# Kernel optimization log

Hardware: AMD Instinct MI355X
Metric: run time of the kernel (lower is better)

The kernel has to match this reference:

```python
import jax, jax.numpy as jnp
import numpy as np

D_MODEL = 2048
NUM_HEADS = 16
HEAD_DIM = D_MODEL // NUM_HEADS
SCALE = HEAD_DIM ** 0.5
B, TQ, CACHE_LEN = 4, 1024, 1024


def setup_inputs() -> dict:
    key = jax.random.key(0)
    ks = jax.random.split(key, 13)
    f = jnp.float32
    inp = {
        'query': jax.random.normal(ks[0], (B, TQ, D_MODEL), f),
        'key': jax.random.normal(ks[1], (B, TQ, D_MODEL), f),
        'value': jax.random.normal(ks[2], (B, TQ, D_MODEL), f),
        'cache_key': jax.random.normal(ks[3], (B, CACHE_LEN, D_MODEL), f),
        'cache_value': jax.random.normal(ks[4], (B, CACHE_LEN, D_MODEL), f),
        'Wq': jax.random.normal(ks[5], (D_MODEL, D_MODEL), f) * 0.02,
        'bq': jnp.zeros((D_MODEL,), f),
        'Wk': jax.random.normal(ks[6], (D_MODEL, D_MODEL), f) * 0.02,
        'bk': jnp.zeros((D_MODEL,), f),
        'Wv': jax.random.normal(ks[7], (D_MODEL, D_MODEL), f) * 0.02,
        'bv': jnp.zeros((D_MODEL,), f),
        'Wo': jax.random.normal(ks[8], (D_MODEL, D_MODEL), f) * 0.02,
        'bo': jnp.zeros((D_MODEL,), f),
    }
    return inp


def _split(x):
    b, t, _ = x.shape
    return jnp.transpose(x.reshape(b, t, NUM_HEADS, HEAD_DIM), (0, 2, 1, 3))  # [B,H,T,Dh]


def reference(query, key, value, cache_key, cache_value, Wq, bq, Wk, bk, Wv, bv, Wo, bo):
    b, tq, _ = query.shape
    Q = query @ Wq.T + bq
    K = key @ Wk.T + bk
    V = value @ Wv.T + bv
    # cache holds already-projected K/V; concat along time
    K = jnp.concatenate([cache_key, K], axis=1)
    V = jnp.concatenate([cache_value, V], axis=1)
    total = K.shape[1]
    Qh, Kh, Vh = _split(Q), _split(K), _split(V)  # [B,H,T,Dh]
    scores = jnp.einsum('bhqd,bhkd->bhqk', Qh, Kh) / SCALE  # [B,H,Tq,total]
    # faithful to original: tril(Tq, total) mask (row i sees cols 0..i)
    mask = jnp.tril(jnp.ones((tq, total), dtype=bool))
    scores = jnp.where(mask[None, None], scores, -jnp.inf)
    attn = jax.nn.softmax(scores, axis=-1)  # eval mode: no dropout
    out = jnp.einsum('bhqk,bhkd->bhqd', attn, Vh)
    out = jnp.transpose(out, (0, 2, 1, 3)).reshape(b, tq, D_MODEL)
    out = out @ Wo.T + bo
    # new cache: torch reshapes the transposed [B,H,T,Dh] tensor directly
    new_k = Kh.reshape(b, -1, D_MODEL)
    new_v = Vh.reshape(b, -1, D_MODEL)
    return out, new_k, new_v
```

## Files before the change

kernel.cpp:

```cpp
#include <hip/hip_runtime.h>
#include <hip/hip_bf16.h>


typedef __bf16 bf16x8 __attribute__((ext_vector_type(8)));
typedef unsigned short u16x8 __attribute__((ext_vector_type(8)));
typedef float  f32x4  __attribute__((ext_vector_type(4)));
typedef unsigned int u32;

#define MFMA16(a, b, c) __builtin_amdgcn_mfma_f32_16x16x32_bf16((a), (b), (c), 0, 0, 0)

__device__ __forceinline__ void async16(__bf16* lds_p, const __bf16* g) {
    __builtin_amdgcn_global_load_lds(
        (__attribute__((address_space(1))) void*)g,
        (__attribute__((address_space(3))) void*)lds_p, 16, 0, 0);
}

__global__ __launch_bounds__(256) void prep(
    const float* __restrict__ q, const float* __restrict__ k, const float* __restrict__ v,
    const float* __restrict__ wq, const float* __restrict__ wk,
    const float* __restrict__ wv, const float* __restrict__ wo,
    const float* __restrict__ ck, const float* __restrict__ cv,
    float* __restrict__ nk, float* __restrict__ nv,
    __bf16* __restrict__ dq, __bf16* __restrict__ dk, __bf16* __restrict__ dv,
    __bf16* __restrict__ dwq, __bf16* __restrict__ dwk,
    __bf16* __restrict__ dwv, __bf16* __restrict__ dwo,
    __bf16* __restrict__ ckb, __bf16* __restrict__ cvb) {
    const int nthreads = gridDim.x * blockDim.x;
    for (int i = blockIdx.x * blockDim.x + threadIdx.x; i < 7340032; i += nthreads) {
        if (i < 2097152) {
            const int sel = i >> 20;
            const int j = i & 1048575;
            const int dh8 = j & 15;
            const int t = (j >> 4) & 1023;
            const int h = (j >> 14) & 15;
            const int b = j >> 18;
            const float* src = sel ? cv : ck;
            float* dst = sel ? nv : nk;
            __bf16* dstb = sel ? cvb : ckb;
            const size_t si = ((size_t)(b << 10) + t) * 2048 + (h << 7) + (dh8 << 3);
            const size_t di = ((size_t)b << 22) + ((size_t)h << 18) + (t << 7) + (dh8 << 3);
            const size_t bi = (((size_t)(b * 16 + h) * 1024 + t) << 7) + (dh8 << 3);
            const f32x4 x0 = *(const f32x4*)&src[si];
            const f32x4 x1 = *(const f32x4*)&src[si + 4];
            *(f32x4*)&dst[di] = x0;
            *(f32x4*)&dst[di + 4] = x1;
            bf16x8 bx;
#pragma unroll
            for (int e = 0; e < 4; e++) {
                bx[e]     = (__bf16)x0[e];
                bx[e + 4] = (__bf16)x1[e];
            }
            *(bf16x8*)&dstb[bi] = bx;
        } else {
            const float* s;
            __bf16* d;
            int off;
            if (i < 5242880) {
                const int ii = i - 2097152;
                const int r = ii >> 20;
                off = ii & 1048575;
                s = (r == 0) ? q : (r == 1) ? k : v;
                d = (r == 0) ? dq : (r == 1) ? dk : dv;
            } else {
                const int ii = i - 5242880;
                const int r = ii >> 19;
                off = ii & 524287;
                s = (r == 0) ? wq : (r == 1) ? wk : (r == 2) ? wv : wo;
                d = (r == 0) ? dwq : (r == 1) ? dwk : (r == 2) ? dwv : dwo;
            }
            const f32x4 x0 = *(const f32x4*)(s + (size_t)off * 8);
            const f32x4 x1 = *(const f32x4*)(s + (size_t)off * 8 + 4);
            bf16x8 o;
#pragma unroll
            for (int j2 = 0; j2 < 4; j2++) {
                o[j2]     = (__bf16)x0[j2];
                o[j2 + 4] = (__bf16)x1[j2];
            }
            *(bf16x8*)(d + (size_t)off * 8) = o;
        }
    }
}

template <int MODE>
__global__ __launch_bounds__(512, 2) void gemm8(
    const __bf16* __restrict__ A,
    const __bf16* __restrict__ W0, const __bf16* __restrict__ W1,
    const __bf16* __restrict__ W2,
    const float* __restrict__ bz0, const float* __restrict__ bz1,
    const float* __restrict__ bz2,
    void* __restrict__ C0, float* __restrict__ C1, float* __restrict__ C2) {
    extern __shared__ __bf16 lds[];
    constexpr int K = 2048;
    const int tid = threadIdx.x;
    const int w = tid >> 6, lane = tid & 63;
    const int wm = w >> 2, wn = w & 3;
    const int g = lane >> 4, c = lane & 15;

    const int lin = blockIdx.x;
    const int nb = lin & 7, mb = lin >> 3;
    const int m0 = mb << 7, n0 = nb << 8;
    const int seg = (MODE == 1) ? (mb >> 5) : 0;
    const __bf16* W = (MODE == 0 || seg == 0) ? W0 : (seg == 1) ? W1 : W2;
    const float* bias = (MODE == 0) ? bz0 : (seg == 0) ? bz0 : (seg == 1) ? bz1 : bz2;

    const __bf16* Ab = A + (size_t)m0 * K;
    const __bf16* Wb = W + (size_t)n0 * K;

    const int srow = lane >> 2;
    const int sch = (lane & 3) ^ (((lane >> 5) & 1) << 1);
    const int foff = c * 32 + ((g ^ ((c >> 3) << 1)) << 3);

    f32x4 acc[4][4] = {};

    auto stgA = [&](int T, int rg) {
#pragma unroll
        for (int u = 0; u < 2; u++) {
            const __bf16* gs = Ab + (size_t)(w * 16 + srow) * K + T * 64 + u * 32 + sch * 8;
            async16(&lds[rg * 24576 + (w * 2 + u) * 512], gs);
        }
    };
    auto stgB = [&](int T, int rg) {
#pragma unroll
        for (int u = 0; u < 4; u++) {
            const int rowblk = 2 * w + (u >> 1), kk = u & 1;
            const __bf16* gs = Wb + (size_t)(rowblk * 16 + srow) * K + T * 64 + kk * 32 + sch * 8;
            async16(&lds[rg * 24576 + 8192 + (w * 4 + u) * 512], gs);
        }
    };

    stgA(0, 0); stgB(0, 0);
    stgA(1, 1); stgB(1, 1);
    asm volatile("s_waitcnt vmcnt(6)" ::: "memory");
    asm volatile("s_barrier" ::: "memory");

    int rg = 0;
    for (int T = 0; T < 32; T++) {
        int rs = rg + 2; if (rs >= 3) rs -= 3;
        const int base = rg * 24576;
        bf16x8 fa[4], fb[4];

#pragma unroll
        for (int mi = 0; mi < 4; mi++)
            fa[mi] = *(const bf16x8*)&lds[base + ((wm * 4 + mi) * 2 + 0) * 512 + foff];
#pragma unroll
        for (int ni = 0; ni < 4; ni++)
            fb[ni] = *(const bf16x8*)&lds[base + 8192 + ((wn * 4 + ni) * 2 + 0) * 512 + foff];
        if (T < 30) stgA(T + 2, rs);
        asm volatile("s_barrier" ::: "memory");
        asm volatile("s_waitcnt lgkmcnt(0)" ::: "memory");
        __builtin_amdgcn_sched_barrier(0);
        __builtin_amdgcn_s_setprio(1);
#pragma unroll
        for (int mi = 0; mi < 4; mi++)
#pragma unroll
            for (int ni = 0; ni < 4; ni++)
                acc[mi][ni] = MFMA16(fa[mi], fb[ni], acc[mi][ni]);
        __builtin_amdgcn_s_setprio(0);
        asm volatile("s_barrier" ::: "memory");

#pragma unroll
        for (int mi = 0; mi < 4; mi++)
            fa[mi] = *(const bf16x8*)&lds[base + ((wm * 4 + mi) * 2 + 1) * 512 + foff];
#pragma unroll
        for (int ni = 0; ni < 4; ni++)
            fb[ni] = *(const bf16x8*)&lds[base + 8192 + ((wn * 4 + ni) * 2 + 1) * 512 + foff];
        if (T < 30) {
            stgB(T + 2, rs);
            asm volatile("s_waitcnt vmcnt(6)" ::: "memory");
        } else {
            asm volatile("s_waitcnt vmcnt(0)" ::: "memory");
        }
        asm volatile("s_barrier" ::: "memory");
        asm volatile("s_waitcnt lgkmcnt(0)" ::: "memory");
        __builtin_amdgcn_sched_barrier(0);
        __builtin_amdgcn_s_setprio(1);
#pragma unroll
        for (int mi = 0; mi < 4; mi++)
#pragma unroll
            for (int ni = 0; ni < 4; ni++)
                acc[mi][ni] = MFMA16(fa[mi], fb[ni], acc[mi][ni]);
        __builtin_amdgcn_s_setprio(0);
        asm volatile("s_barrier" ::: "memory");

        rg = (rg + 1 == 3) ? 0 : rg + 1;
    }

#pragma unroll
    for (int ni = 0; ni < 4; ni++) {
        const int col = n0 + wn * 64 + ni * 16 + c;
        const float bv = bias[col];
        const int h = col >> 7, dh = col & 127;
#pragma unroll
        for (int mi = 0; mi < 4; mi++) {
            const int rowb = m0 + wm * 64 + mi * 16 + g * 4;
#pragma unroll
            for (int r = 0; r < 4; r++) {
                const float v = acc[mi][ni][r] + bv;
                if (MODE == 0) {
                    ((float*)C0)[(size_t)(rowb + r) * 2048 + col] = v;
                } else {
                    const int lrow = (rowb + r) & 4095;
                    const int b = lrow >> 10, t = lrow & 1023;
                    if (seg == 0)
                        ((__bf16*)C0)[(((size_t)(b * 16 + h) * 1024) + t) * 128 + dh] = (__bf16)v;
                    else if (seg == 1)
                        C1[(((size_t)(b * 16 + h) * 2048) + 1024 + t) * 128 + dh] = v;
                    else
                        C2[(((size_t)(b * 16 + h) * 2048) + 1024 + t) * 128 + dh] = v;
                }
            }
        }
    }
}

__global__ __launch_bounds__(128) void attn_k(const __bf16* __restrict__ Qw,
                                              const __bf16* __restrict__ cK,
                                              const __bf16* __restrict__ cV,
                                              __bf16* __restrict__ O) {
    __shared__ __bf16 Kt[32 * 128];
    __shared__ u32 Vt32[128 * 16];
    __shared__ __bf16 Pw[2][16 * 32];

    const int tid = threadIdx.x;
    const int w = tid >> 6;
    const int lane = tid & 63;
    const int g = lane >> 4, c = lane & 15;

    const int lin = blockIdx.x + (blockIdx.y << 4) + (blockIdx.z << 8);
    const int xcd = lin & 7;
    const int j = lin >> 3;
    const int bh = xcd * 8 + (j & 7);
    const int qq = j >> 3;
    const int c4 = qq & 3, m = qq >> 2;
    const int qb = ((m & 1) == 0) ? (c4 * 4 + (m >> 1)) : (31 - c4 * 4 - (m >> 1));
    const int b = bh >> 4, h = bh & 15;
    const int q0 = qb << 5;
    const float inv_scale = 0.08838834764831845f;

    const __bf16* qbase = Qw + (((size_t)bh * 1024) + q0 + w * 16) * 128;
    bf16x8 qf[4];
#pragma unroll
    for (int dc = 0; dc < 4; dc++)
        qf[dc] = *(const bf16x8*)&qbase[c * 128 + dc * 32 + g * 8];

    f32x4 accO[8] = {};
    float m_run[4], l_run[4];
#pragma unroll
    for (int r = 0; r < 4; r++) { m_run[r] = -1e30f; l_run[r] = 0.0f; }

    const int trips = qb + 1;
    const __bf16* kb = cK + (size_t)bh * 1024 * 128;
    const __bf16* vb = cV + (size_t)bh * 1024 * 128;

    const int skey = tid >> 2, sgrp = tid & 3;
    const int ss = skey & 7;
    const int kp = tid >> 3, dbv = tid & 7;

    for (int kt = 0; kt < trips; kt++) {
        const int k0 = kt * 32;
        const __bf16* kr = &kb[(size_t)(k0 + skey) * 128 + sgrp * 32];
        const bf16x8 k_a = *(const bf16x8*)&kr[0];
        const bf16x8 k_b = *(const bf16x8*)&kr[8];
        const bf16x8 k_c = *(const bf16x8*)&kr[16];
        const bf16x8 k_d = *(const bf16x8*)&kr[24];
        const __bf16* vr0 = &vb[(size_t)(k0 + 2 * kp) * 128 + dbv * 16];
        const __bf16* vr1 = &vb[(size_t)(k0 + 2 * kp + 1) * 128 + dbv * 16];
        const bf16x8 v0a = *(const bf16x8*)&vr0[0];
        const bf16x8 v0b = *(const bf16x8*)&vr0[8];
        const bf16x8 v1a = *(const bf16x8*)&vr1[0];
        const bf16x8 v1b = *(const bf16x8*)&vr1[8];
        __syncthreads();
        {
            const int c0 = sgrp * 4;
            *(bf16x8*)&Kt[skey * 128 + (((c0 + 0) ^ ss) << 3)] = k_a;
            *(bf16x8*)&Kt[skey * 128 + (((c0 + 1) ^ ss) << 3)] = k_b;
            *(bf16x8*)&Kt[skey * 128 + (((c0 + 2) ^ ss) << 3)] = k_c;
            *(bf16x8*)&Kt[skey * 128 + (((c0 + 3) ^ ss) << 3)] = k_d;
        }
        {
            const u16x8 a0 = __builtin_bit_cast(u16x8, v0a);
            const u16x8 a1 = __builtin_bit_cast(u16x8, v0b);
            const u16x8 b0 = __builtin_bit_cast(u16x8, v1a);
            const u16x8 b1 = __builtin_bit_cast(u16x8, v1b);
#pragma unroll
            for (int jj = 0; jj < 8; jj++) {
                const int d0 = dbv * 16 + jj;
                const int d1 = dbv * 16 + 8 + jj;
                const int pc0 = (((kp >> 2) ^ ((d0 >> 3) & 3)) << 2) | (kp & 3);
                const int pc1 = (((kp >> 2) ^ ((d1 >> 3) & 3)) << 2) | (kp & 3);
                Vt32[d0 * 16 + pc0] = (u32)a0[jj] | ((u32)b0[jj] << 16);
                Vt32[d1 * 16 + pc1] = (u32)a1[jj] | ((u32)b1[jj] << 16);
            }
        }
        __syncthreads();

        f32x4 s_acc[2] = {};
#pragma unroll
        for (int nt = 0; nt < 2; nt++) {
            const int krow = nt * 16 + c;
            const int ks = krow & 7;
#pragma unroll
            for (int dc = 0; dc < 4; dc++) {
                const bf16x8 kf =
                    *(const bf16x8*)&Kt[krow * 128 + (((dc * 4 + g) ^ ks) << 3)];
                s_acc[nt] = MFMA16(qf[dc], kf, s_acc[nt]);
            }
        }

        float p[2][4], alpha[4];
#pragma unroll
        for (int r = 0; r < 4; r++) {
            const int qrow = q0 + w * 16 + g * 4 + r;
            float s0 = (k0 + c      <= qrow) ? s_acc[0][r] * inv_scale : -1e30f;
            float s1 = (k0 + 16 + c <= qrow) ? s_acc[1][r] * inv_scale : -1e30f;
            float rm = fmaxf(s0, s1);
            rm = fmaxf(rm, __shfl_xor(rm, 1));
            rm = fmaxf(rm, __shfl_xor(rm, 2));
            rm = fmaxf(rm, __shfl_xor(rm, 4));
            rm = fmaxf(rm, __shfl_xor(rm, 8));
            const float mnew = fmaxf(m_run[r], rm);
            alpha[r] = __expf(m_run[r] - mnew);
            const float p0 = __expf(s0 - mnew);
            const float p1 = __expf(s1 - mnew);
            p[0][r] = p0; p[1][r] = p1;
            float ps = p0 + p1;
            ps += __shfl_xor(ps, 1);
            ps += __shfl_xor(ps, 2);
            ps += __shfl_xor(ps, 4);
            ps += __shfl_xor(ps, 8);
            l_run[r] = alpha[r] * l_run[r] + ps;
            m_run[r] = mnew;
        }
#pragma unroll
        for (int nt2 = 0; nt2 < 8; nt2++)
#pragma unroll
            for (int r = 0; r < 4; r++)
                accO[nt2][r] *= alpha[r];

#pragma unroll
        for (int nt = 0; nt < 2; nt++)
#pragma unroll
            for (int r = 0; r < 4; r++)
                Pw[w][(g * 4 + r) * 32 + ((((nt << 1) | (c >> 3)) ^ g) << 3) + (c & 7)] =
                    (__bf16)p[nt][r];
        asm volatile("s_waitcnt lgkmcnt(0)" ::: "memory");
        __builtin_amdgcn_sched_barrier(0);

        const bf16x8 pf = *(const bf16x8*)&Pw[w][c * 32 + ((g ^ ((c >> 2) & 3)) << 3)];
#pragma unroll
        for (int nt2 = 0; nt2 < 8; nt2++) {
            const int vrow = nt2 * 16 + c;
            const bf16x8 vf = *(const bf16x8*)&(
                (const __bf16*)Vt32)[vrow * 32 + ((g ^ ((vrow >> 3) & 3)) << 3)];
            accO[nt2] = MFMA16(pf, vf, accO[nt2]);
        }
    }

#pragma unroll
    for (int nt2 = 0; nt2 < 8; nt2++)
#pragma unroll
        for (int r = 0; r < 4; r++) {
            const float v = accO[nt2][r] / l_run[r];
            const int row = b * 1024 + q0 + w * 16 + g * 4 + r;
            const int col = h * 128 + nt2 * 16 + c;
            O[(size_t)row * 2048 + col] = (__bf16)v;
        }
}

extern "C" void kernel_launch(void* const* d_in, const int* in_sizes, int n_in,
                              void* d_out, int out_size, void* d_ws, size_t ws_size,
                              hipStream_t stream) {
    const float* query       = (const float*)d_in[0];
    const float* key         = (const float*)d_in[1];
    const float* value       = (const float*)d_in[2];
    const float* cache_key   = (const float*)d_in[3];
    const float* cache_value = (const float*)d_in[4];
    const float* Wq = (const float*)d_in[5];
    const float* bq = (const float*)d_in[6];
    const float* Wk = (const float*)d_in[7];
    const float* bk = (const float*)d_in[8];
    const float* Wv = (const float*)d_in[9];
    const float* bv = (const float*)d_in[10];
    const float* Wo = (const float*)d_in[11];
    const float* bo = (const float*)d_in[12];

    float* out   = (float*)d_out;
    float* new_k = out + 8388608;
    float* new_v = out + 25165824;

    __bf16* p = (__bf16*)d_ws;
    __bf16* ws_q    = p; p += 8388608;
    __bf16* ws_attn = p; p += 8388608;
    __bf16* q_bf    = p; p += 8388608;
    __bf16* k_bf    = p; p += 8388608;
    __bf16* v_bf    = p; p += 8388608;
    __bf16* wq_bf   = p; p += 4194304;
    __bf16* wk_bf   = p; p += 4194304;
    __bf16* wv_bf   = p; p += 4194304;
    __bf16* wo_bf   = p; p += 4194304;
    __bf16* ck_bf   = p; p += 8388608;
    __bf16* cv_bf   = p;

    static bool s_attr = false;
    if (!s_attr) {
        hipFuncSetAttribute(reinterpret_cast<const void*>(&gemm8<1>),
                            hipFuncAttributeMaxDynamicSharedMemorySize, 147456);
        hipFuncSetAttribute(reinterpret_cast<const void*>(&gemm8<0>),
                            hipFuncAttributeMaxDynamicSharedMemorySize, 147456);
        s_attr = true;
    }

    prep<<<4096, 256, 0, stream>>>(query, key, value, Wq, Wk, Wv, Wo,
                                   cache_key, cache_value, new_k, new_v,
                                   q_bf, k_bf, v_bf, wq_bf, wk_bf, wv_bf, wo_bf,
                                   ck_bf, cv_bf);
    gemm8<1><<<768, 512, 147456, stream>>>(q_bf, wq_bf, wk_bf, wv_bf,
                                           bq, bk, bv, ws_q, new_k, new_v);
    attn_k<<<dim3(16, 16, 8), 128, 0, stream>>>(ws_q, ck_bf, cv_bf, ws_attn);
    gemm8<0><<<256, 512, 147456, stream>>>(ws_attn, wo_bf, nullptr, nullptr,
                                           bo, nullptr, nullptr, out, nullptr, nullptr);
}
```

Baseline: 617.9 us.

## Load K tiles via direct global-to-LDS and prefetch next V tile in registers

The attention kernel now copies K tiles straight from global memory into LDS with async global_load_lds. The XOR swizzle moves onto the source address so the LDS writes stay contiguous per wave. V for the next key tile is loaded into registers during the current tile's compute, overlapping global latency with the MFMAs. The V transpose swizzle is also changed to a new hash to reduce LDS bank conflicts. The risks are higher register pressure and relying on the compiler's waitcnt placement for the async LDS loads.

```diff
diff --git a/kernel.cpp b/kernel.cpp
--- a/kernel.cpp
+++ b/kernel.cpp
@@ -231,8 +231,8 @@
     const int j = lin >> 3;
     const int bh = xcd * 8 + (j & 7);
     const int qq = j >> 3;
-    const int c4 = qq & 3, m = qq >> 2;
-    const int qb = ((m & 1) == 0) ? (c4 * 4 + (m >> 1)) : (31 - c4 * 4 - (m >> 1));
+    const int c4 = qq & 3, mq = qq >> 2;
+    const int qb = ((mq & 1) == 0) ? (c4 * 4 + (mq >> 1)) : (31 - c4 * 4 - (mq >> 1));
     const int b = bh >> 4, h = bh & 15;
     const int q0 = qb << 5;
     const float inv_scale = 0.08838834764831845f;
@@ -252,31 +252,30 @@
     const __bf16* kb = cK + (size_t)bh * 1024 * 128;
     const __bf16* vb = cV + (size_t)bh * 1024 * 128;
 
-    const int skey = tid >> 2, sgrp = tid & 3;
-    const int ss = skey & 7;
+    size_t ksrc[4];
+    __bf16* kdst[4];
+#pragma unroll
+    for (int j2 = 0; j2 < 4; j2++) {
+        const int keyb = w * 16 + j2 * 4;
+        const int row = keyb + (lane >> 4);
+        ksrc[j2] = (size_t)row * 128 + (((lane & 15) ^ (row & 7)) << 3);
+        kdst[j2] = &Kt[keyb * 128];
+    }
+
     const int kp = tid >> 3, dbv = tid & 7;
+    const __bf16* vbase = vb + (size_t)(2 * kp) * 128 + dbv * 16;
+
+    bf16x8 v0a = *(const bf16x8*)&vbase[0];
+    bf16x8 v0b = *(const bf16x8*)&vbase[8];
+    bf16x8 v1a = *(const bf16x8*)&vbase[128];
+    bf16x8 v1b = *(const bf16x8*)&vbase[136];
 
     for (int kt = 0; kt < trips; kt++) {
         const int k0 = kt * 32;
-        const __bf16* kr = &kb[(size_t)(k0 + skey) * 128 + sgrp * 32];
-        const bf16x8 k_a = *(const bf16x8*)&kr[0];
-        const bf16x8 k_b = *(const bf16x8*)&kr[8];
-        const bf16x8 k_c = *(const bf16x8*)&kr[16];
-        const bf16x8 k_d = *(const bf16x8*)&kr[24];
-        const __bf16* vr0 = &vb[(size_t)(k0 + 2 * kp) * 128 + dbv * 16];
-        const __bf16* vr1 = &vb[(size_t)(k0 + 2 * kp + 1) * 128 + dbv * 16];
-        const bf16x8 v0a = *(const bf16x8*)&vr0[0];
-        const bf16x8 v0b = *(const bf16x8*)&vr0[8];
-        const bf16x8 v1a = *(const bf16x8*)&vr1[0];
-        const bf16x8 v1b = *(const bf16x8*)&vr1[8];
         __syncthreads();
-        {
-            const int c0 = sgrp * 4;
-            *(bf16x8*)&Kt[skey * 128 + (((c0 + 0) ^ ss) << 3)] = k_a;
-            *(bf16x8*)&Kt[skey * 128 + (((c0 + 1) ^ ss) << 3)] = k_b;
-            *(bf16x8*)&Kt[skey * 128 + (((c0 + 2) ^ ss) << 3)] = k_c;
-            *(bf16x8*)&Kt[skey * 128 + (((c0 + 3) ^ ss) << 3)] = k_d;
-        }
+#pragma unroll
+        for (int j2 = 0; j2 < 4; j2++)
+            async16(kdst[j2], kb + (size_t)k0 * 128 + ksrc[j2]);
         {
             const u16x8 a0 = __builtin_bit_cast(u16x8, v0a);
             const u16x8 a1 = __builtin_bit_cast(u16x8, v0b);
@@ -285,14 +284,26 @@
 #pragma unroll
             for (int jj = 0; jj < 8; jj++) {
                 const int d0 = dbv * 16 + jj;
-                const int d1 = dbv * 16 + 8 + jj;
-                const int pc0 = (((kp >> 2) ^ ((d0 >> 3) & 3)) << 2) | (kp & 3);
-                const int pc1 = (((kp >> 2) ^ ((d1 >> 3) & 3)) << 2) | (kp & 3);
-                Vt32[d0 * 16 + pc0] = (u32)a0[jj] | ((u32)b0[jj] << 16);
-                Vt32[d1 * 16 + pc1] = (u32)a1[jj] | ((u32)b1[jj] << 16);
+                const int d1 = d0 + 8;
+                const int h0 = ((d0 >> 4) ^ (d0 >> 2)) & 3;
+                const int h1 = ((d1 >> 4) ^ (d1 >> 2)) & 3;
+                const int col0 = (((kp >> 2) ^ h0) << 2) | (kp & 3);
+                const int col1 = (((kp >> 2) ^ h1) << 2) | (kp & 3);
+                Vt32[d0 * 16 + col0] = (u32)a0[jj] | ((u32)b0[jj] << 16);
+                Vt32[d1 * 16 + col1] = (u32)a1[jj] | ((u32)b1[jj] << 16);
             }
         }
         __syncthreads();
+
+        const bool more = (kt + 1 < trips);
+        bf16x8 n0a = {}, n0b = {}, n1a = {}, n1b = {};
+        if (more) {
+            const __bf16* vn = vbase + (size_t)(k0 + 32) * 128;
+            n0a = *(const bf16x8*)&vn[0];
+            n0b = *(const bf16x8*)&vn[8];
+            n1a = *(const bf16x8*)&vn[128];
+            n1b = *(const bf16x8*)&vn[136];
+        }
 
         f32x4 s_acc[2] = {};
 #pragma unroll
@@ -350,10 +361,13 @@
 #pragma unroll
         for (int nt2 = 0; nt2 < 8; nt2++) {
             const int vrow = nt2 * 16 + c;
+            const int hv = ((vrow >> 4) ^ (vrow >> 2)) & 3;
             const bf16x8 vf = *(const bf16x8*)&(
-                (const __bf16*)Vt32)[vrow * 32 + ((g ^ ((vrow >> 3) & 3)) << 3)];
+                (const __bf16*)Vt32)[vrow * 32 + ((g ^ hv) << 3)];
             accO[nt2] = MFMA16(pf, vf, accO[nt2]);
         }
+
+        if (more) { v0a = n0a; v0b = n0b; v1a = n1a; v1b = n1b; }
     }
 
 #pragma unroll
```

New measurement: 622.1 us. Within noise of the previous version (+0.7%).
